# Optimization experiments

Hardware: AMD Instinct MI355X
Metric: run time of the kernel (lower is better)

The kernel has to match this reference:

```python
import jax, jax.numpy as jnp
import numpy as np

DIM = 64
MIN_HZ = 0.5
MAX_HZ = 3.5
T = 262144  # number of consecutive samples (n_samples)


def setup_inputs() -> dict:
    key = jax.random.key(0)
    k1, k2 = jax.random.split(key)
    # instantaneous bin probabilities (rows sum to 1, like a softmax output)
    ps = jax.random.uniform(k1, (T, DIM), dtype=jnp.float32)
    ps = ps / jnp.sum(ps, axis=1, keepdims=True)
    # transition prior matrix (fit_layer would produce a dense positive matrix)
    transition_prior = jax.random.uniform(k2, (DIM, DIM), dtype=jnp.float32) + 1e-3
    # bins[i] = hr(i) = min_hz*60 + (max_hz-min_hz)*60*i/dim
    bins = MIN_HZ * 60.0 + (MAX_HZ - MIN_HZ) * 60.0 * jnp.arange(DIM, dtype=jnp.float32) / DIM
    # initial state: uniform belief 1/dim
    state = jnp.ones((DIM,), dtype=jnp.float32) / DIM
    return {"ps": ps, "transition_prior": transition_prior, "bins": bins, "state": state}


def reference(ps, transition_prior, bins, state):
    # online sum-product message passing (is_online=True):
    #   p_prior = T @ state ; p_new = p_prior * ps[i] ; state = p_new / sum(p_new)
    def step(s, p):
        p_new = (transition_prior @ s) * p
        s_new = p_new / jnp.sum(p_new)
        return s_new, s_new

    _, probs = jax.lax.scan(step, state, ps)  # probs: (T, DIM)

    # return_probs=False -> expected HR in BPM + entropy uncertainty
    E_x = probs @ bins                                   # (T,)
    uncert = -jnp.sum(probs * jnp.log(probs + 1e-10), axis=1)  # (T,)
    return (E_x, uncert)
```

## Files before the change

kernel.cpp:

```cpp
#include <hip/hip_runtime.h>

#define DIM 64
#define CHUNK 64
#define WARM 16
#define GSTR 16
#define RSTRIDE 68
#define NROW 16

typedef float v2f __attribute__((ext_vector_type(2)));
typedef float v4f __attribute__((ext_vector_type(4)));

__device__ __forceinline__ float dpp_add_xor1(float x) {
    int y = __builtin_amdgcn_update_dpp(0, __float_as_int(x), 0xB1 , 0xF, 0xF, true);
    return x + __int_as_float(y);
}
__device__ __forceinline__ float dpp_add_xor2(float x) {
    int y = __builtin_amdgcn_update_dpp(0, __float_as_int(x), 0x4E , 0xF, 0xF, true);
    return x + __int_as_float(y);
}

__global__ __launch_bounds__(64, 4) void prior_layer_kernel(
    const float* __restrict__ ps,
    const float* __restrict__ tp,
    const float* __restrict__ state0,
    float* __restrict__ out,
    int T)
{
    __shared__ __align__(16) float uhist[NROW * RSTRIDE];
    const int L  = threadIdx.x;
    const int kg = L & 3;
    const int jq = L >> 2;
    const bool lb0 = (L & 1) != 0;
    const bool lb1 = (L & 2) != 0;

    const int nwg = gridDim.x;
    const int bid = blockIdx.x;
    const int c = ((nwg & 7) == 0) ? ((bid & 7) * (nwg >> 3) + (bid >> 3)) : bid;

    const long t_begin = (long)c * CHUNK;
    if (t_begin >= T) return;
    const int warm = (t_begin > 0) ? WARM : 0;
    const long tstart = t_begin - warm;
    int nout = (int)(T - t_begin); if (nout > CHUNK) nout = CHUNK;
    const int warmblk = warm / NROW;
    const int nblk = (nout + NROW - 1) / NROW;
    const int totblk = warmblk + nblk;

    v2f Trow[4][8];
    {
        const float* tpb = tp + (4 * jq) * DIM + 16 * kg;
#pragma unroll
        for (int m = 0; m < 4; ++m)
#pragma unroll
            for (int g = 0; g < 4; ++g) {
                v4f x = *(const v4f*)(tpb + m * DIM + 4 * g);
                Trow[m][2 * g]     = (v2f){2.0f * x.x, 2.0f * x.y};
                Trow[m][2 * g + 1] = (v2f){2.0f * x.z, 2.0f * x.w};
            }
    }

    uhist[(NROW - 1) * RSTRIDE + L] = state0[L];

    const float* pp = ps + tstart * DIM + L;
    const float* const pplast = ps + (long)(T - 1) * DIM + L;
    float psq[8];
#pragma unroll
    for (int q = 0; q < 8; ++q) {
        const float* pl = pp < pplast ? pp : pplast;
        psq[q] = *pl;
        pp += DIM;
    }

    const float* prev = &uhist[(NROW - 1) * RSTRIDE];

    for (int bn = 0; bn < totblk; ++bn) {
        for (int rb = 0; rb < NROW; rb += 8) {
            float* base = &uhist[rb * RSTRIDE];
#pragma unroll
            for (int q = 0; q < 8; ++q) {
                const float* rsrc = (q == 0) ? prev : (base + (q - 1) * RSTRIDE);
                const v4f* s4 = (const v4f*)(rsrc + GSTR * kg);
                v4f x0 = s4[0], x1 = s4[1], x2 = s4[2], x3 = s4[3];
                v2f p0 = {x0.x, x0.y}, p1 = {x0.z, x0.w};
                v2f p2 = {x1.x, x1.y}, p3 = {x1.z, x1.w};
                v2f p4 = {x2.x, x2.y}, p5 = {x2.z, x2.w};
                v2f p6 = {x3.x, x3.y}, p7 = {x3.z, x3.w};
                float t0, t1, t2, t3;
#pragma unroll
                for (int m = 0; m < 4; ++m) {
                    v2f a = Trow[m][0] * p0;
                    a = __builtin_elementwise_fma(Trow[m][1], p1, a);
                    a = __builtin_elementwise_fma(Trow[m][2], p2, a);
                    a = __builtin_elementwise_fma(Trow[m][3], p3, a);
                    a = __builtin_elementwise_fma(Trow[m][4], p4, a);
                    a = __builtin_elementwise_fma(Trow[m][5], p5, a);
                    a = __builtin_elementwise_fma(Trow[m][6], p6, a);
                    a = __builtin_elementwise_fma(Trow[m][7], p7, a);
                    float s = a.x + a.y;
                    s = dpp_add_xor1(s);
                    s = dpp_add_xor2(s);
                    if (m == 0) t0 = s; else if (m == 1) t1 = s;
                    else if (m == 2) t2 = s; else t3 = s;
                }
                float r01 = lb0 ? t1 : t0;
                float r23 = lb0 ? t3 : t2;
                float u = (lb1 ? r23 : r01) * psq[q];
                base[q * RSTRIDE + L] = u;
                const float* pl = pp < pplast ? pp : pplast;
                psq[q] = *pl;
                pp += DIM;
            }
            prev = base + 7 * RSTRIDE;
        }

        if (bn >= warmblk) {
            const int ob = bn - warmblk;
            const long tb = t_begin + (long)ob * NROW;
            int valid = nout - ob * NROW; if (valid > NROW) valid = NROW;

            const int s  = L & 15;
            const int kq = L >> 4;
            const v4f* src = (const v4f*)&uhist[s * RSTRIDE + 16 * kq];
            v2f S2 = {0.f, 0.f}, M2 = {0.f, 0.f};
            float H0 = 0.f, H1 = 0.f;
#pragma unroll
            for (int g = 0; g < 4; ++g) {
                v4f x = src[g];
                float kb = (float)(16 * kq + 4 * g);
                v2f lo = {x.x, x.y}, hi = {x.z, x.w};
                S2 += lo + hi;
                M2 = __builtin_elementwise_fma(lo, (v2f){kb, kb + 1.f}, M2);
                M2 = __builtin_elementwise_fma(hi, (v2f){kb + 2.f, kb + 3.f}, M2);
                H0 = fmaf(x.x, __log2f(x.x + 1e-35f), H0);
                H1 = fmaf(x.y, __log2f(x.y + 1e-35f), H1);
                H0 = fmaf(x.z, __log2f(x.z + 1e-35f), H0);
                H1 = fmaf(x.w, __log2f(x.w + 1e-35f), H1);
            }
            float Sl = S2.x + S2.y;
            float Ml = M2.x + M2.y;
            float Hl = H0 + H1;
            Sl += __shfl_xor(Sl, 16, 64);  Sl += __shfl_xor(Sl, 32, 64);
            Ml += __shfl_xor(Ml, 16, 64);  Ml += __shfl_xor(Ml, 32, 64);
            Hl += __shfl_xor(Hl, 16, 64);  Hl += __shfl_xor(Hl, 32, 64);
            float rinv = 1.0f / Sl;
            float E = fmaf(2.8125f * rinv, Ml, 30.0f);
            float ent = 0.6931471805599453f * fmaf(-rinv, Hl, __log2f(Sl));
            if (L < valid) {
                out[tb + L] = E;
                out[(long)T + tb + L] = ent;
            }
        }
    }
}

extern "C" void kernel_launch(void* const* d_in, const int* in_sizes, int n_in,
                              void* d_out, int out_size, void* d_ws, size_t ws_size,
                              hipStream_t stream)
{
    const float* ps    = (const float*)d_in[0];
    const float* tp    = (const float*)d_in[1];
    const float* st    = (const float*)d_in[3];
    float* out = (float*)d_out;

    const int T = in_sizes[0] / DIM;
    const int C = (T + CHUNK - 1) / CHUNK;
    prior_layer_kernel<<<C, DIM, 0, stream>>>(ps, tp, st, out, T);
}
```

Before: 125.3 us.

## Interleave two independent chunk recurrences per workgroup to hide latency

Each workgroup now runs two independent chunks (A and B) in lockstep, interleaving their matvec steps so that one chunk's dependent chain of LDS reads, FMAs and DPP reductions can overlap the other's. Chunk 0 goes to a separate single-chain block. The grid is roughly halved and the occupancy hint is dropped from launch bounds. The DPP adds are written as inline asm so each becomes a single v_add_f32_dpp, and address clamping uses unsigned byte offsets with min. The code assumes T is a multiple of CHUNK and that the chunk count is even, and it hardcodes the block counts for warmup plus output.

```diff
diff --git a/kernel.cpp b/kernel.cpp
--- a/kernel.cpp
+++ b/kernel.cpp
@@ -11,40 +11,99 @@
 typedef float v4f __attribute__((ext_vector_type(4)));
 
 __device__ __forceinline__ float dpp_add_xor1(float x) {
-    int y = __builtin_amdgcn_update_dpp(0, __float_as_int(x), 0xB1 , 0xF, 0xF, true);
-    return x + __int_as_float(y);
+    float r;
+    asm("v_add_f32_dpp %0, %1, %2 quad_perm:[1,0,3,2] row_mask:0xf bank_mask:0xf"
+        : "=v"(r) : "v"(x), "v"(x));
+    return r;
 }
 __device__ __forceinline__ float dpp_add_xor2(float x) {
-    int y = __builtin_amdgcn_update_dpp(0, __float_as_int(x), 0x4E , 0xF, 0xF, true);
-    return x + __int_as_float(y);
-}
-
-__global__ __launch_bounds__(64, 4) void prior_layer_kernel(
+    float r;
+    asm("v_add_f32_dpp %0, %1, %2 quad_perm:[2,3,0,1] row_mask:0xf bank_mask:0xf"
+        : "=v"(r) : "v"(x), "v"(x));
+    return r;
+}
+
+#define QSTEP(prevp, basep, psq, boff, qq) do {                                \
+    const v4f* s4_ = (const v4f*)((prevp) + GSTR * kg);                        \
+    v4f x0_ = s4_[0], x1_ = s4_[1], x2_ = s4_[2], x3_ = s4_[3];                \
+    v2f p0_ = {x0_.x, x0_.y}, p1_ = {x0_.z, x0_.w};                            \
+    v2f p2_ = {x1_.x, x1_.y}, p3_ = {x1_.z, x1_.w};                            \
+    v2f p4_ = {x2_.x, x2_.y}, p5_ = {x2_.z, x2_.w};                            \
+    v2f p6_ = {x3_.x, x3_.y}, p7_ = {x3_.z, x3_.w};                            \
+    float t0_, t1_, t2_, t3_;                                                  \
+    _Pragma("unroll")                                                          \
+    for (int m_ = 0; m_ < 4; ++m_) {                                           \
+        v2f a_ = Trow[m_][0] * p0_;                                            \
+        a_ = __builtin_elementwise_fma(Trow[m_][1], p1_, a_);                  \
+        a_ = __builtin_elementwise_fma(Trow[m_][2], p2_, a_);                  \
+        a_ = __builtin_elementwise_fma(Trow[m_][3], p3_, a_);                  \
+        a_ = __builtin_elementwise_fma(Trow[m_][4], p4_, a_);                  \
+        a_ = __builtin_elementwise_fma(Trow[m_][5], p5_, a_);                  \
+        a_ = __builtin_elementwise_fma(Trow[m_][6], p6_, a_);                  \
+        a_ = __builtin_elementwise_fma(Trow[m_][7], p7_, a_);                  \
+        float s_ = a_.x + a_.y;                                                \
+        s_ = dpp_add_xor1(s_);                                                 \
+        s_ = dpp_add_xor2(s_);                                                 \
+        if (m_ == 0) t0_ = s_; else if (m_ == 1) t1_ = s_;                     \
+        else if (m_ == 2) t2_ = s_; else t3_ = s_;                             \
+    }                                                                          \
+    float r01_ = lb0 ? t1_ : t0_;                                              \
+    float r23_ = lb0 ? t3_ : t2_;                                              \
+    float u_ = (lb1 ? r23_ : r01_) * (psq)[qq];                                \
+    (basep)[(qq) * RSTRIDE + L] = u_;                                          \
+    (psq)[qq] = *(const float*)((const char*)ps + (boff));                     \
+    (boff) = min((boff) + 256u, boffmax);                                      \
+} while (0)
+
+#define PHASE2(uhp, tb) do {                                                   \
+    const int s_ = L & 15;                                                     \
+    const int kq_ = L >> 4;                                                    \
+    const v4f* src_ = (const v4f*)&(uhp)[s_ * RSTRIDE + 16 * kq_];             \
+    v2f S2_ = {0.f, 0.f}, M2_ = {0.f, 0.f};                                    \
+    float H0_ = 0.f, H1_ = 0.f;                                                \
+    _Pragma("unroll")                                                          \
+    for (int g_ = 0; g_ < 4; ++g_) {                                           \
+        v4f x_ = src_[g_];                                                     \
+        float kb_ = (float)(16 * kq_ + 4 * g_);                                \
+        v2f lo_ = {x_.x, x_.y}, hi_ = {x_.z, x_.w};                            \
+        S2_ += lo_ + hi_;                                                      \
+        M2_ = __builtin_elementwise_fma(lo_, (v2f){kb_, kb_ + 1.f}, M2_);      \
+        M2_ = __builtin_elementwise_fma(hi_, (v2f){kb_ + 2.f, kb_ + 3.f}, M2_);\
+        H0_ = fmaf(x_.x, __log2f(x_.x + 1e-35f), H0_);                         \
+        H1_ = fmaf(x_.y, __log2f(x_.y + 1e-35f), H1_);                         \
+        H0_ = fmaf(x_.z, __log2f(x_.z + 1e-35f), H0_);                         \
+        H1_ = fmaf(x_.w, __log2f(x_.w + 1e-35f), H1_);                         \
+    }                                                                          \
+    float Sl_ = S2_.x + S2_.y;                                                 \
+    float Ml_ = M2_.x + M2_.y;                                                 \
+    float Hl_ = H0_ + H1_;                                                     \
+    Sl_ += __shfl_xor(Sl_, 16, 64);  Sl_ += __shfl_xor(Sl_, 32, 64);           \
+    Ml_ += __shfl_xor(Ml_, 16, 64);  Ml_ += __shfl_xor(Ml_, 32, 64);           \
+    Hl_ += __shfl_xor(Hl_, 16, 64);  Hl_ += __shfl_xor(Hl_, 32, 64);           \
+    float rinv_ = 1.0f / Sl_;                                                  \
+    float E_ = fmaf(2.8125f * rinv_, Ml_, 30.0f);                              \
+    float ent_ = 0.6931471805599453f * fmaf(-rinv_, Hl_, __log2f(Sl_));        \
+    if (L < NROW) {                                                            \
+        outE[(tb) + L] = E_;                                                   \
+        outU[(tb) + L] = ent_;                                                 \
+    }                                                                          \
+} while (0)
+
+__global__ __launch_bounds__(64) void prior_layer_kernel(
     const float* __restrict__ ps,
     const float* __restrict__ tp,
     const float* __restrict__ state0,
     float* __restrict__ out,
     int T)
 {
-    __shared__ __align__(16) float uhist[NROW * RSTRIDE];
+    __shared__ __align__(16) float uh[2][NROW * RSTRIDE];
     const int L  = threadIdx.x;
     const int kg = L & 3;
     const int jq = L >> 2;
     const bool lb0 = (L & 1) != 0;
     const bool lb1 = (L & 2) != 0;
-
-    const int nwg = gridDim.x;
-    const int bid = blockIdx.x;
-    const int c = ((nwg & 7) == 0) ? ((bid & 7) * (nwg >> 3) + (bid >> 3)) : bid;
-
-    const long t_begin = (long)c * CHUNK;
-    if (t_begin >= T) return;
-    const int warm = (t_begin > 0) ? WARM : 0;
-    const long tstart = t_begin - warm;
-    int nout = (int)(T - t_begin); if (nout > CHUNK) nout = CHUNK;
-    const int warmblk = warm / NROW;
-    const int nblk = (nout + NROW - 1) / NROW;
-    const int totblk = warmblk + nblk;
+    const int NCH = T / CHUNK;
+    const int NDUAL = NCH / 2;
 
     v2f Trow[4][8];
     {
@@ -59,96 +118,73 @@
             }
     }
 
-    uhist[(NROW - 1) * RSTRIDE + L] = state0[L];
-
-    const float* pp = ps + tstart * DIM + L;
-    const float* const pplast = ps + (long)(T - 1) * DIM + L;
-    float psq[8];
-#pragma unroll
-    for (int q = 0; q < 8; ++q) {
-        const float* pl = pp < pplast ? pp : pplast;
-        psq[q] = *pl;
-        pp += DIM;
-    }
-
-    const float* prev = &uhist[(NROW - 1) * RSTRIDE];
-
-    for (int bn = 0; bn < totblk; ++bn) {
-        for (int rb = 0; rb < NROW; rb += 8) {
-            float* base = &uhist[rb * RSTRIDE];
-#pragma unroll
-            for (int q = 0; q < 8; ++q) {
-                const float* rsrc = (q == 0) ? prev : (base + (q - 1) * RSTRIDE);
-                const v4f* s4 = (const v4f*)(rsrc + GSTR * kg);
-                v4f x0 = s4[0], x1 = s4[1], x2 = s4[2], x3 = s4[3];
-                v2f p0 = {x0.x, x0.y}, p1 = {x0.z, x0.w};
-                v2f p2 = {x1.x, x1.y}, p3 = {x1.z, x1.w};
-                v2f p4 = {x2.x, x2.y}, p5 = {x2.z, x2.w};
-                v2f p6 = {x3.x, x3.y}, p7 = {x3.z, x3.w};
-                float t0, t1, t2, t3;
-#pragma unroll
-                for (int m = 0; m < 4; ++m) {
-                    v2f a = Trow[m][0] * p0;
-                    a = __builtin_elementwise_fma(Trow[m][1], p1, a);
-                    a = __builtin_elementwise_fma(Trow[m][2], p2, a);
-                    a = __builtin_elementwise_fma(Trow[m][3], p3, a);
-                    a = __builtin_elementwise_fma(Trow[m][4], p4, a);
-                    a = __builtin_elementwise_fma(Trow[m][5], p5, a);
-                    a = __builtin_elementwise_fma(Trow[m][6], p6, a);
-                    a = __builtin_elementwise_fma(Trow[m][7], p7, a);
-                    float s = a.x + a.y;
-                    s = dpp_add_xor1(s);
-                    s = dpp_add_xor2(s);
-                    if (m == 0) t0 = s; else if (m == 1) t1 = s;
-                    else if (m == 2) t2 = s; else t3 = s;
+    const unsigned boffmax = ((unsigned)(T - 1) * DIM + (unsigned)L) * 4u;
+    float* outE = out;
+    float* outU = out + T;
+    const float s0v = state0[L];
+
+    if ((int)blockIdx.x < NDUAL) {
+        const int w  = blockIdx.x;
+        const int wp = ((NDUAL & 7) == 0) ? ((w & 7) * (NDUAL >> 3) + (w >> 3)) : w;
+        const int cA = 1 + wp;
+        int cB = NDUAL + 1 + wp; if (cB > NCH - 1) cB = NCH - 1;
+        const long tbA = (long)cA * CHUNK, tbB = (long)cB * CHUNK;
+        float* uhA = uh[0];
+        float* uhB = uh[1];
+        uhA[(NROW - 1) * RSTRIDE + L] = s0v;
+        uhB[(NROW - 1) * RSTRIDE + L] = s0v;
+        unsigned boffA = (unsigned)((tbA - WARM) * DIM + L) * 4u;
+        unsigned boffB = (unsigned)((tbB - WARM) * DIM + L) * 4u;
+        float psqA[8], psqB[8];
+#pragma unroll
+        for (int q = 0; q < 8; ++q) {
+            psqA[q] = *(const float*)((const char*)ps + boffA); boffA += 256u;
+            psqB[q] = *(const float*)((const char*)ps + boffB); boffB += 256u;
+        }
+        const float* prevA = &uhA[(NROW - 1) * RSTRIDE];
+        const float* prevB = &uhB[(NROW - 1) * RSTRIDE];
+
+        for (int bn = 0; bn < 5; ++bn) {
+            for (int rb = 0; rb < NROW; rb += 8) {
+                float* baseA = &uhA[rb * RSTRIDE];
+                float* baseB = &uhB[rb * RSTRIDE];
+#pragma unroll
+                for (int q = 0; q < 8; ++q) {
+                    const float* pA_ = (q == 0) ? prevA : (baseA + (q - 1) * RSTRIDE);
+                    const float* pB_ = (q == 0) ? prevB : (baseB + (q - 1) * RSTRIDE);
+                    QSTEP(pA_, baseA, psqA, boffA, q);
+                    QSTEP(pB_, baseB, psqB, boffB, q);
                 }
-                float r01 = lb0 ? t1 : t0;
-                float r23 = lb0 ? t3 : t2;
-                float u = (lb1 ? r23 : r01) * psq[q];
-                base[q * RSTRIDE + L] = u;
-                const float* pl = pp < pplast ? pp : pplast;
-                psq[q] = *pl;
-                pp += DIM;
-            }
-            prev = base + 7 * RSTRIDE;
-        }
-
-        if (bn >= warmblk) {
-            const int ob = bn - warmblk;
-            const long tb = t_begin + (long)ob * NROW;
-            int valid = nout - ob * NROW; if (valid > NROW) valid = NROW;
-
-            const int s  = L & 15;
-            const int kq = L >> 4;
-            const v4f* src = (const v4f*)&uhist[s * RSTRIDE + 16 * kq];
-            v2f S2 = {0.f, 0.f}, M2 = {0.f, 0.f};
-            float H0 = 0.f, H1 = 0.f;
-#pragma unroll
-            for (int g = 0; g < 4; ++g) {
-                v4f x = src[g];
-                float kb = (float)(16 * kq + 4 * g);
-                v2f lo = {x.x, x.y}, hi = {x.z, x.w};
-                S2 += lo + hi;
-                M2 = __builtin_elementwise_fma(lo, (v2f){kb, kb + 1.f}, M2);
-                M2 = __builtin_elementwise_fma(hi, (v2f){kb + 2.f, kb + 3.f}, M2);
-                H0 = fmaf(x.x, __log2f(x.x + 1e-35f), H0);
-                H1 = fmaf(x.y, __log2f(x.y + 1e-35f), H1);
-                H0 = fmaf(x.z, __log2f(x.z + 1e-35f), H0);
-                H1 = fmaf(x.w, __log2f(x.w + 1e-35f), H1);
-            }
-            float Sl = S2.x + S2.y;
-            float Ml = M2.x + M2.y;
-            float Hl = H0 + H1;
-            Sl += __shfl_xor(Sl, 16, 64);  Sl += __shfl_xor(Sl, 32, 64);
-            Ml += __shfl_xor(Ml, 16, 64);  Ml += __shfl_xor(Ml, 32, 64);
-            Hl += __shfl_xor(Hl, 16, 64);  Hl += __shfl_xor(Hl, 32, 64);
-            float rinv = 1.0f / Sl;
-            float E = fmaf(2.8125f * rinv, Ml, 30.0f);
-            float ent = 0.6931471805599453f * fmaf(-rinv, Hl, __log2f(Sl));
-            if (L < valid) {
-                out[tb + L] = E;
-                out[(long)T + tb + L] = ent;
-            }
+                prevA = baseA + 7 * RSTRIDE;
+                prevB = baseB + 7 * RSTRIDE;
+            }
+            if (bn >= 1) {
+                const long ob = (long)(bn - 1) * NROW;
+                PHASE2(uhA, tbA + ob);
+                PHASE2(uhB, tbB + ob);
+            }
+        }
+    } else {
+        float* uhA = uh[0];
+        uhA[(NROW - 1) * RSTRIDE + L] = s0v;
+        unsigned boffA = (unsigned)L * 4u;
+        float psqA[8];
+#pragma unroll
+        for (int q = 0; q < 8; ++q) {
+            psqA[q] = *(const float*)((const char*)ps + boffA); boffA += 256u;
+        }
+        const float* prevA = &uhA[(NROW - 1) * RSTRIDE];
+        for (int bn = 0; bn < 4; ++bn) {
+            for (int rb = 0; rb < NROW; rb += 8) {
+                float* baseA = &uhA[rb * RSTRIDE];
+#pragma unroll
+                for (int q = 0; q < 8; ++q) {
+                    const float* pA_ = (q == 0) ? prevA : (baseA + (q - 1) * RSTRIDE);
+                    QSTEP(pA_, baseA, psqA, boffA, q);
+                }
+                prevA = baseA + 7 * RSTRIDE;
+            }
+            PHASE2(uhA, (long)bn * NROW);
         }
     }
 }
@@ -163,6 +199,7 @@
     float* out = (float*)d_out;
 
     const int T = in_sizes[0] / DIM;
-    const int C = (T + CHUNK - 1) / CHUNK;
-    prior_layer_kernel<<<C, DIM, 0, stream>>>(ps, tp, st, out, T);
-}
+    const int NCH = T / CHUNK;
+    const int grid = NCH / 2 + 1;
+    prior_layer_kernel<<<grid, DIM, 0, stream>>>(ps, tp, st, out, T);
+}
```

New measurement: 123.8 us. About the same (-1.2%).
